# Kernel optimization log

Hardware: AMD Instinct MI355X
Metric: run time of the kernel (lower is better)

## Reference

```python
import jax, jax.numpy as jnp
import numpy as np

ZDIM, NF, H, S, B = 64, 32, 256, 256, 1024


def setup_inputs() -> dict:
    key = jax.random.key(0)
    ks = jax.random.split(key, 8)
    def w(k, shape, fan):
        return (jax.random.normal(k, shape, jnp.float32) / np.sqrt(fan)).astype(jnp.float32)
    return {
        "z": jax.random.normal(ks[0], (B, ZDIM), jnp.float32),
        "W_lat": w(ks[1], (2 * H, ZDIM), ZDIM),
        "b_lat": jnp.zeros((2 * H,), jnp.float32),
        "W_ih": w(ks[2], (4 * H, NF), NF),
        "b_ih": jnp.zeros((4 * H,), jnp.float32),
        "W_hh": w(ks[3], (4 * H, H), H),
        "b_hh": jnp.zeros((4 * H,), jnp.float32),
        "W_out": w(ks[4], (NF, H), H),
        "b_out": jnp.zeros((NF,), jnp.float32),
        "W_sig": w(ks[5], (NF, H * S), H * S),
        "b_sig": jnp.zeros((NF,), jnp.float32),
    }


def reference(z, W_lat, b_lat, W_ih, b_ih, W_hh, b_hh, W_out, b_out, W_sig, b_sig):
    # from_latent: split into initial hidden / cell state
    hc = z @ W_lat.T + b_lat                      # [B, 2H]
    h, c = hc[:, :H], hc[:, H:]
    x = jnp.zeros((z.shape[0], NF), z.dtype)      # initial LSTM input
    bias = b_ih + b_hh                            # fold both LSTM biases

    def step(carry, _):
        h, c, x = carry
        g = x @ W_ih.T + h @ W_hh.T + bias        # [B, 4H]; torch gate order i,f,g,o
        i, f, gg, o = jnp.split(g, 4, axis=-1)
        c = jax.nn.sigmoid(f) * c + jax.nn.sigmoid(i) * jnp.tanh(gg)
        h = jax.nn.sigmoid(o) * jnp.tanh(c)
        x_next = jnp.tanh(h) @ W_out.T + b_out    # activation(Tanh) then from_lstm
        return (h, c, x_next), (h, x_next)

    _, (hs, mus) = jax.lax.scan(step, (h, c, x), None, length=S)
    # mus: [S, B, NF] -> mu: [B, NF, S]
    mu = jnp.transpose(mus, (1, 2, 0))
    # hs: [S, B, H] -> [B, H, S] -> flatten hidden-major, matching torch permute+reshape
    xs = jnp.transpose(hs, (1, 2, 0)).reshape(-1, H * S)
    sigma = jax.nn.softplus(xs @ W_sig.T + b_sig)[:, :, None]   # [B, NF, 1]
    return (mu, sigma)
```

## Files before the change

kernel.cpp:

```cpp
#include <hip/hip_runtime.h>

#define ZDIM 64
#define NF 32
#define HDIM 256
#define SLEN 256
#define BATCH 1024

typedef float f32x4 __attribute__((ext_vector_type(4)));
typedef __bf16 bf16x8 __attribute__((ext_vector_type(8)));

#define MFMA __builtin_amdgcn_mfma_f32_16x16x32_bf16

#define WHH_O 0
#define WIH_O 32768
#define WOUT_O 36864
#define WLAT_O 37888
#define PREP1_N 41984
#define WT_BYTE (1 << 20)
#define HST_BYTE (8 << 20)

__device__ __forceinline__ unsigned short f2bf(float x) {
  union { float f; unsigned int u; } v; v.f = x;
  unsigned int r = (v.u + 0x7FFFu + ((v.u >> 16) & 1u)) >> 16;
  return (unsigned short)r;
}
__device__ __forceinline__ unsigned int pk2(float a, float b) {
  return (unsigned int)f2bf(a) | ((unsigned int)f2bf(b) << 16);
}
__device__ __forceinline__ float sigf(float x) {
  return __fdividef(1.0f, 1.0f + __expf(-x));
}
__device__ __forceinline__ float tanhf_(float x) {
  return 1.0f - __fdividef(2.0f, __expf(2.0f * x) + 1.0f);
}

__global__ void prep_weights(const float* __restrict__ Whh, const float* __restrict__ Wih,
                             const float* __restrict__ Wout, const float* __restrict__ Wlat,
                             uint4* __restrict__ ws) {
  int i = blockIdx.x * 256 + threadIdx.x;
  if (i >= PREP1_N) return;
  int l = i & 63;
  int c16 = l & 15, g4 = l >> 4;
  const float* src;
  if (i < WIH_O) {
    int t = (i >> 6) & 7, j = i >> 9;
    src = Whh + (j * 16 + c16) * 256 + t * 32 + 8 * g4;
  } else if (i < WOUT_O) {
    int ii = i - WIH_O;
    int j = ii >> 6;
    src = Wih + (j * 16 + c16) * 32 + 8 * g4;
  } else if (i < WLAT_O) {
    int ii = i - WOUT_O;
    int t = (ii >> 6) & 7, j = ii >> 9;
    src = Wout + (j * 16 + c16) * 256 + t * 32 + 8 * g4;
  } else {
    int ii = i - WLAT_O;
    int t = (ii >> 6) & 1, j = ii >> 7;
    src = Wlat + (j * 16 + c16) * 64 + t * 32 + 8 * g4;
  }
  uint4 P;
  P.x = pk2(src[0], src[1]);
  P.y = pk2(src[2], src[3]);
  P.z = pk2(src[4], src[5]);
  P.w = pk2(src[6], src[7]);
  ws[i] = P;
}

__global__ void prep_wt(const float* __restrict__ Wsig, unsigned short* __restrict__ Wt) {
  __shared__ float tile[32][257];
  int f = blockIdx.x >> 3, hb = blockIdx.x & 7;
  int tid = threadIdx.x;
  const float* src = Wsig + f * (HDIM * SLEN) + hb * 32 * 256;
#pragma unroll
  for (int i = 0; i < 32; ++i) {
    tile[i][tid] = src[i * 256 + tid];
  }
  __syncthreads();
  int s = tid;
  unsigned short tmp[32];
#pragma unroll
  for (int h = 0; h < 32; ++h) tmp[h] = f2bf(tile[h][s]);
  uint4* dst = (uint4*)(Wt + f * 65536 + s * 256 + hb * 32);
  const uint4* tsrc = (const uint4*)tmp;
#pragma unroll
  for (int j = 0; j < 4; ++j) dst[j] = tsrc[j];
}

__global__ __launch_bounds__(512) void lstm_scan(
    const float* __restrict__ z, const float* __restrict__ b_lat,
    const float* __restrict__ b_ih, const float* __restrict__ b_hh,
    const float* __restrict__ b_out,
    const uint4* __restrict__ ws, unsigned short* __restrict__ hst,
    float* __restrict__ out) {
  __shared__ __align__(16) uint4 wihb[4096];
  __shared__ __align__(16) uint4 woutb[1024];
  __shared__ __align__(16) unsigned short hbuf[2][16][256];
  __shared__ __align__(16) unsigned short thbuf[16][256];
  __shared__ __align__(16) unsigned short xbuf[2][16][32];
  __shared__ __align__(16) float mubuf[16][16][32];
  __shared__ __align__(16) unsigned short zb[16][64];

  const int tid = threadIdx.x;
  const int w = tid >> 6;
  const int l = tid & 63;
  const int c16 = l & 15;
  const int g4 = l >> 4;
  const int r0 = g4 * 4;
  const int wg = blockIdx.x;

  for (int i = tid; i < 4096; i += 512) wihb[i] = ws[WIH_O + i];
  for (int i = tid; i < 1024; i += 512) woutb[i] = ws[WOUT_O + i];

  float biasv[8];
#pragma unroll
  for (int q = 0; q < 8; ++q) {
    int n = (q * 8 + w) * 16 + c16;
    biasv[q] = b_ih[n] + b_hh[n];
  }
  float bo = 0.f;
  if (w < 2) bo = b_out[w * 16 + c16];

  for (int idx = tid; idx < 16 * 64; idx += 512) {
    int m = idx >> 6, k = idx & 63;
    zb[m][k] = f2bf(z[(wg * 16 + m) * 64 + k]);
  }
  xbuf[0][tid >> 5][tid & 31] = 0;
  __syncthreads();

  float cst[2][4];
  {
    bf16x8 za0 = *reinterpret_cast<const bf16x8*>(&zb[c16][8 * g4]);
    bf16x8 za1 = *reinterpret_cast<const bf16x8*>(&zb[c16][32 + 8 * g4]);
    f32x4 a2[4];
#pragma unroll
    for (int q2 = 0; q2 < 4; ++q2) {
      int j = q2 * 8 + w;
      float bl = b_lat[j * 16 + c16];
      f32x4 a = {bl, bl, bl, bl};
      a = MFMA(za0, *reinterpret_cast<const bf16x8*>(ws + WLAT_O + (j * 2 + 0) * 64 + l), a, 0, 0, 0);
      a = MFMA(za1, *reinterpret_cast<const bf16x8*>(ws + WLAT_O + (j * 2 + 1) * 64 + l), a, 0, 0, 0);
      a2[q2] = a;
    }
#pragma unroll
    for (int q2 = 0; q2 < 2; ++q2) {
      int col = q2 * 128 + w * 16 + c16;
#pragma unroll
      for (int v = 0; v < 4; ++v) {
        int rr = r0 + v;
        hbuf[0][rr][col ^ ((rr & 7) << 3)] = f2bf(a2[q2][v]);
      }
    }
#pragma unroll
    for (int p = 0; p < 2; ++p)
#pragma unroll
      for (int v = 0; v < 4; ++v) cst[p][v] = a2[2 + p][v];
  }
  __syncthreads();

  for (int s = 0; s < SLEN; ++s) {
    const int pb = s & 1;
    bf16x8 afr[8];
#pragma unroll
    for (int t = 0; t < 8; ++t) {
      int kb = t * 32 + 8 * g4;
      afr[t] = *reinterpret_cast<const bf16x8*>(&hbuf[pb][c16][kb ^ ((c16 & 7) << 3)]);
    }
    bf16x8 xfr = *reinterpret_cast<const bf16x8*>(&xbuf[pb][c16][8 * g4]);
    f32x4 acc[8];
#pragma unroll
    for (int q = 0; q < 8; ++q) {
      f32x4 a = {biasv[q], biasv[q], biasv[q], biasv[q]};
      a = MFMA(xfr, *reinterpret_cast<const bf16x8*>(&wihb[(q * 8 + w) * 64 + l]), a, 0, 0, 0);
      const uint4* bp = ws + WHH_O + ((q * 8 + w) * 8) * 64 + l;
#pragma unroll
      for (int t = 0; t < 8; ++t)
        a = MFMA(afr[t], *reinterpret_cast<const bf16x8*>(bp + t * 64), a, 0, 0, 0);
      acc[q] = a;
    }

#pragma unroll
    for (int p = 0; p < 2; ++p) {
      const int hcol = p * 128 + w * 16 + c16;
#pragma unroll
      for (int v = 0; v < 4; ++v) {
        float iv = acc[0 + p][v];
        float fv = acc[2 + p][v];
        float gv = acc[4 + p][v];
        float ov = acc[6 + p][v];
        float cc = sigf(fv) * cst[p][v] + sigf(iv) * tanhf_(gv);
        cst[p][v] = cc;
        float hh = sigf(ov) * tanhf_(cc);
        float th = tanhf_(hh);
        int rr = r0 + v;
        int sc = hcol ^ ((rr & 7) << 3);
        hbuf[pb ^ 1][rr][sc] = f2bf(hh);
        thbuf[rr][sc] = f2bf(th);
      }
    }
    __syncthreads();
    if (w < 2) {
      f32x4 xacc = {bo, bo, bo, bo};
#pragma unroll
      for (int t = 0; t < 8; ++t) {
        bf16x8 ta = *reinterpret_cast<const bf16x8*>(
            &thbuf[c16][(t * 32 + 8 * g4) ^ ((c16 & 7) << 3)]);
        xacc = MFMA(ta, *reinterpret_cast<const bf16x8*>(&woutb[(w * 8 + t) * 64 + l]), xacc, 0, 0, 0);
      }
      const int f = w * 16 + c16;
      const int sw = s & 15;
#pragma unroll
      for (int v = 0; v < 4; ++v) {
        int rr = r0 + v;
        float xv = xacc[v];
        xbuf[pb ^ 1][rr][f] = f2bf(xv);
        mubuf[sw][rr][f] = xv;
      }
    } else if (w >= 4) {
      int t4 = tid - 256;
#pragma unroll
      for (int rep = 0; rep < 2; ++rep) {
        int task = t4 + rep * 256;
        int r = task >> 5;
        int h0 = (task & 31) * 8;
        uint4 d = *reinterpret_cast<const uint4*>(&hbuf[pb ^ 1][r][h0 ^ ((r & 7) << 3)]);
        *reinterpret_cast<uint4*>(hst + ((wg * 16 + r) << 16) + (s << 8) + h0) = d;
      }
    }
    __syncthreads();
    if ((s & 15) == 15) {
      int b = tid >> 5, f = tid & 31;
      float* dst = out + ((wg * 16 + b) << 13) + (f << 8) + (s - 15);
#pragma unroll
      for (int j4 = 0; j4 < 4; ++j4) {
        f32x4 vv;
#pragma unroll
        for (int jj = 0; jj < 4; ++jj) vv[jj] = mubuf[j4 * 4 + jj][b][f];
        *reinterpret_cast<f32x4*>(dst + j4 * 4) = vv;
      }
    }
  }
}

__global__ __launch_bounds__(512) void sigma_gemm(
    const unsigned short* __restrict__ hst, const unsigned short* __restrict__ Wt,
    const float* __restrict__ b_sig, float* __restrict__ out) {
  __shared__ float sred[8][16][32];
  const int tid = threadIdx.x;
  const int w = tid >> 6;
  const int l = tid & 63;
  const int c16 = l & 15;
  const int g4 = l >> 4;
  const int wg = blockIdx.x;

  const unsigned short* ap =
      hst + (((wg << 2) + (c16 & 3)) << 16) + ((w * 32) << 8) + (g4 << 3);
  const unsigned short* bp0 = Wt + (c16 << 16) + ((w * 32) << 8) + (g4 << 3);
  const unsigned short* bp1 = Wt + ((16 + c16) << 16) + ((w * 32) << 8) + (g4 << 3);

  f32x4 a0 = {0.f, 0.f, 0.f, 0.f}, a1 = {0.f, 0.f, 0.f, 0.f};
#pragma unroll 8
  for (int kk = 0; kk < 256; ++kk) {
    int off = ((kk >> 3) << 8) + ((kk & 7) << 5);
    bf16x8 av = *reinterpret_cast<const bf16x8*>(ap + off);
    a0 = MFMA(av, *reinterpret_cast<const bf16x8*>(bp0 + off), a0, 0, 0, 0);
    a1 = MFMA(av, *reinterpret_cast<const bf16x8*>(bp1 + off), a1, 0, 0, 0);
  }
#pragma unroll
  for (int v = 0; v < 4; ++v) {
    sred[w][g4 * 4 + v][c16] = a0[v];
    sred[w][g4 * 4 + v][16 + c16] = a1[v];
  }
  __syncthreads();
  int b = tid >> 5, f = tid & 31;
  if (b < 4) {
    float acc = b_sig[f];
#pragma unroll
    for (int ww = 0; ww < 8; ++ww) acc += sred[ww][b][f];
    float sp = fmaxf(acc, 0.0f) + log1pf(__expf(-fabsf(acc)));
    out[BATCH * NF * SLEN + ((wg << 2) + b) * NF + f] = sp;
  }
}

extern "C" void kernel_launch(void* const* d_in, const int* in_sizes, int n_in,
                              void* d_out, int out_size, void* d_ws, size_t ws_size,
                              hipStream_t stream) {
  (void)in_sizes; (void)n_in; (void)out_size; (void)ws_size;
  const float* z     = (const float*)d_in[0];
  const float* W_lat = (const float*)d_in[1];
  const float* b_lat = (const float*)d_in[2];
  const float* W_ih  = (const float*)d_in[3];
  const float* b_ih  = (const float*)d_in[4];
  const float* W_hh  = (const float*)d_in[5];
  const float* b_hh  = (const float*)d_in[6];
  const float* W_out = (const float*)d_in[7];
  const float* b_out = (const float*)d_in[8];
  const float* W_sig = (const float*)d_in[9];
  const float* b_sig = (const float*)d_in[10];
  uint4* ws = (uint4*)d_ws;
  unsigned short* Wt  = (unsigned short*)((char*)d_ws + WT_BYTE);
  unsigned short* hst = (unsigned short*)((char*)d_ws + HST_BYTE);
  float* out = (float*)d_out;

  prep_weights<<<(PREP1_N + 255) / 256, 256, 0, stream>>>(W_hh, W_ih, W_out, W_lat, ws);
  prep_wt<<<256, 256, 0, stream>>>(W_sig, Wt);
  lstm_scan<<<64, 512, 0, stream>>>(z, b_lat, b_ih, b_hh, b_out, ws, hst, out);
  sigma_gemm<<<256, 512, 0, stream>>>(hst, Wt, b_sig, out);
}
```

Baseline: 3.255 ms.

## Keep W_hh resident in registers and LDS, prefetch the remainder from global

Repartitions the recurrent weight W_hh per wave: three gate tiles are pinned in VGPRs, two are staged in LDS, and the remaining three are streamed from global memory with software prefetch overlapping the MFMAs. The LDS previously used for W_ih/W_out staging and the mu staging buffer is freed, so W_ih and W_out are now read from global each step and mu is written straight to the output with strided scalar stores. The aim is to cut the per-step global/L2 traffic for W_hh on the latency-bound serial scan. The cost is heavy register pressure, which the launch_bounds(512,2) hint tightens further, plus less coalesced mu stores.

Measured after the change: 3.485 ms. +7.1%, slower.

```diff
diff --git a/kernel.cpp b/kernel.cpp
--- a/kernel.cpp
+++ b/kernel.cpp
@@ -1,6 +1,5 @@
 #include <hip/hip_runtime.h>
 
-#define ZDIM 64
 #define NF 32
 #define HDIM 256
 #define SLEN 256
@@ -8,6 +7,8 @@
 
 typedef float f32x4 __attribute__((ext_vector_type(4)));
 typedef __bf16 bf16x8 __attribute__((ext_vector_type(8)));
+typedef unsigned int u32x4 __attribute__((ext_vector_type(4)));
+typedef unsigned short u16;
 
 #define MFMA __builtin_amdgcn_mfma_f32_16x16x32_bf16
 
@@ -16,13 +17,12 @@
 #define WOUT_O 36864
 #define WLAT_O 37888
 #define PREP1_N 41984
-#define WT_BYTE (1 << 20)
-#define HST_BYTE (8 << 20)
-
-__device__ __forceinline__ unsigned short f2bf(float x) {
+#define WT_BYTE (1u << 20)
+#define HST_BYTE (8u << 20)
+
+__device__ __forceinline__ u16 f2bf(float x) {
   union { float f; unsigned int u; } v; v.f = x;
-  unsigned int r = (v.u + 0x7FFFu + ((v.u >> 16) & 1u)) >> 16;
-  return (unsigned short)r;
+  return (u16)((v.u + 0x7FFFu + ((v.u >> 16) & 1u)) >> 16);
 }
 __device__ __forceinline__ unsigned int pk2(float a, float b) {
   return (unsigned int)f2bf(a) | ((unsigned int)f2bf(b) << 16);
@@ -72,9 +72,7 @@
   int tid = threadIdx.x;
   const float* src = Wsig + f * (HDIM * SLEN) + hb * 32 * 256;
 #pragma unroll
-  for (int i = 0; i < 32; ++i) {
-    tile[i][tid] = src[i * 256 + tid];
-  }
+  for (int i = 0; i < 32; ++i) tile[i][tid] = src[i * 256 + tid];
   __syncthreads();
   int s = tid;
   unsigned short tmp[32];
@@ -86,30 +84,38 @@
   for (int j = 0; j < 4; ++j) dst[j] = tsrc[j];
 }
 
-__global__ __launch_bounds__(512) void lstm_scan(
+__global__ __launch_bounds__(512, 2) void lstm_scan(
     const float* __restrict__ z, const float* __restrict__ b_lat,
     const float* __restrict__ b_ih, const float* __restrict__ b_hh,
     const float* __restrict__ b_out,
     const uint4* __restrict__ ws, unsigned short* __restrict__ hst,
     float* __restrict__ out) {
-  __shared__ __align__(16) uint4 wihb[4096];
-  __shared__ __align__(16) uint4 woutb[1024];
-  __shared__ __align__(16) unsigned short hbuf[2][16][256];
-  __shared__ __align__(16) unsigned short thbuf[16][256];
-  __shared__ __align__(16) unsigned short xbuf[2][16][32];
-  __shared__ __align__(16) float mubuf[16][16][32];
-  __shared__ __align__(16) unsigned short zb[16][64];
-
-  const int tid = threadIdx.x;
-  const int w = tid >> 6;
-  const int l = tid & 63;
-  const int c16 = l & 15;
-  const int g4 = l >> 4;
-  const int r0 = g4 * 4;
+  __shared__ __align__(16) uint4 whhl[8192];
+  __shared__ __align__(16) u16 hbuf[2][16][256];
+  __shared__ __align__(16) u16 thbuf[16][256];
+  __shared__ __align__(16) u16 xbuf[2][16][32];
+
+  const int tid = threadIdx.x, w = tid >> 6, l = tid & 63;
+  const int c16 = l & 15, g4 = l >> 4, r0 = g4 * 4;
   const int wg = blockIdx.x;
-
-  for (int i = tid; i < 4096; i += 512) wihb[i] = ws[WIH_O + i];
-  for (int i = tid; i < 1024; i += 512) woutb[i] = ws[WOUT_O + i];
+  const int swz = (c16 & 7) << 3;
+
+  for (int i = tid; i < 8192; i += 512) {
+    int l_ = i & 63, kt = (i >> 6) & 7, qq = (i >> 9) & 1, w_ = i >> 10;
+    whhl[i] = ws[WHH_O + (((4 + qq) * 8 + w_) * 8 + kt) * 64 + l_];
+  }
+
+  u32x4 wp[3][8];
+#pragma unroll
+  for (int qi = 0; qi < 3; ++qi)
+#pragma unroll
+    for (int kt = 0; kt < 8; ++kt)
+      wp[qi][kt] = __builtin_bit_cast(u32x4, ws[WHH_O + ((qi * 8 + w) * 8 + kt) * 64 + l]);
+#pragma unroll
+  for (int qi = 0; qi < 3; ++qi)
+#pragma unroll
+    for (int kt = 0; kt < 8; ++kt)
+      asm volatile("" : "+v"(wp[qi][kt]));
 
   float biasv[8];
 #pragma unroll
@@ -117,20 +123,17 @@
     int n = (q * 8 + w) * 16 + c16;
     biasv[q] = b_ih[n] + b_hh[n];
   }
-  float bo = 0.f;
-  if (w < 2) bo = b_out[w * 16 + c16];
-
-  for (int idx = tid; idx < 16 * 64; idx += 512) {
-    int m = idx >> 6, k = idx & 63;
-    zb[m][k] = f2bf(z[(wg * 16 + m) * 64 + k]);
-  }
+  float bo = (w < 2) ? b_out[w * 16 + c16] : 0.f;
+
+  for (int idx = tid; idx < 1024; idx += 512)
+    thbuf[idx >> 6][idx & 63] = f2bf(z[(wg * 16 + (idx >> 6)) * 64 + (idx & 63)]);
   xbuf[0][tid >> 5][tid & 31] = 0;
   __syncthreads();
 
   float cst[2][4];
   {
-    bf16x8 za0 = *reinterpret_cast<const bf16x8*>(&zb[c16][8 * g4]);
-    bf16x8 za1 = *reinterpret_cast<const bf16x8*>(&zb[c16][32 + 8 * g4]);
+    bf16x8 za0 = *reinterpret_cast<const bf16x8*>(&thbuf[c16][8 * g4]);
+    bf16x8 za1 = *reinterpret_cast<const bf16x8*>(&thbuf[c16][32 + 8 * g4]);
     f32x4 a2[4];
 #pragma unroll
     for (int q2 = 0; q2 < 4; ++q2) {
@@ -157,26 +160,55 @@
   }
   __syncthreads();
 
+  const uint4* bs3 = ws + WHH_O + ((3 * 8 + w) * 8) * 64 + l;
+  const uint4* bs6 = ws + WHH_O + ((6 * 8 + w) * 8) * 64 + l;
+  const uint4* bs7 = ws + WHH_O + ((7 * 8 + w) * 8) * 64 + l;
+
   for (int s = 0; s < SLEN; ++s) {
     const int pb = s & 1;
-    bf16x8 afr[8];
-#pragma unroll
-    for (int t = 0; t < 8; ++t) {
-      int kb = t * 32 + 8 * g4;
-      afr[t] = *reinterpret_cast<const bf16x8*>(&hbuf[pb][c16][kb ^ ((c16 & 7) << 3)]);
+    uint4 pf[12];
+#pragma unroll
+    for (int kt = 0; kt < 4; ++kt) {
+      pf[kt * 3 + 0] = bs3[kt * 64];
+      pf[kt * 3 + 1] = bs6[kt * 64];
+      pf[kt * 3 + 2] = bs7[kt * 64];
+    }
+    f32x4 acc[8];
+#pragma unroll
+    for (int q = 0; q < 8; ++q) acc[q] = (f32x4){biasv[q], biasv[q], biasv[q], biasv[q]};
+#pragma unroll
+    for (int kt = 0; kt < 8; ++kt) {
+      bf16x8 afr = *reinterpret_cast<const bf16x8*>(&hbuf[pb][c16][(kt * 32 + 8 * g4) ^ swz]);
+      acc[0] = MFMA(afr, __builtin_bit_cast(bf16x8, wp[0][kt]), acc[0], 0, 0, 0);
+      acc[1] = MFMA(afr, __builtin_bit_cast(bf16x8, wp[1][kt]), acc[1], 0, 0, 0);
+      acc[2] = MFMA(afr, __builtin_bit_cast(bf16x8, wp[2][kt]), acc[2], 0, 0, 0);
+      acc[4] = MFMA(afr, *reinterpret_cast<const bf16x8*>(&whhl[((w * 2 + 0) * 8 + kt) * 64 + l]), acc[4], 0, 0, 0);
+      acc[5] = MFMA(afr, *reinterpret_cast<const bf16x8*>(&whhl[((w * 2 + 1) * 8 + kt) * 64 + l]), acc[5], 0, 0, 0);
+    }
+    bf16x8 wihv[8];
+#pragma unroll
+    for (int q = 0; q < 8; ++q)
+      wihv[q] = *reinterpret_cast<const bf16x8*>(ws + WIH_O + (q * 8 + w) * 64 + l);
+#pragma unroll
+    for (int kt = 0; kt < 4; ++kt) {
+      bf16x8 afr = *reinterpret_cast<const bf16x8*>(&hbuf[pb][c16][(kt * 32 + 8 * g4) ^ swz]);
+      acc[3] = MFMA(afr, __builtin_bit_cast(bf16x8, pf[kt * 3 + 0]), acc[3], 0, 0, 0);
+      acc[6] = MFMA(afr, __builtin_bit_cast(bf16x8, pf[kt * 3 + 1]), acc[6], 0, 0, 0);
+      acc[7] = MFMA(afr, __builtin_bit_cast(bf16x8, pf[kt * 3 + 2]), acc[7], 0, 0, 0);
+      pf[kt * 3 + 0] = bs3[(4 + kt) * 64];
+      pf[kt * 3 + 1] = bs6[(4 + kt) * 64];
+      pf[kt * 3 + 2] = bs7[(4 + kt) * 64];
+    }
+#pragma unroll
+    for (int kt = 4; kt < 8; ++kt) {
+      bf16x8 afr = *reinterpret_cast<const bf16x8*>(&hbuf[pb][c16][(kt * 32 + 8 * g4) ^ swz]);
+      acc[3] = MFMA(afr, __builtin_bit_cast(bf16x8, pf[(kt - 4) * 3 + 0]), acc[3], 0, 0, 0);
+      acc[6] = MFMA(afr, __builtin_bit_cast(bf16x8, pf[(kt - 4) * 3 + 1]), acc[6], 0, 0, 0);
+      acc[7] = MFMA(afr, __builtin_bit_cast(bf16x8, pf[(kt - 4) * 3 + 2]), acc[7], 0, 0, 0);
     }
     bf16x8 xfr = *reinterpret_cast<const bf16x8*>(&xbuf[pb][c16][8 * g4]);
-    f32x4 acc[8];
-#pragma unroll
-    for (int q = 0; q < 8; ++q) {
-      f32x4 a = {biasv[q], biasv[q], biasv[q], biasv[q]};
-      a = MFMA(xfr, *reinterpret_cast<const bf16x8*>(&wihb[(q * 8 + w) * 64 + l]), a, 0, 0, 0);
-      const uint4* bp = ws + WHH_O + ((q * 8 + w) * 8) * 64 + l;
-#pragma unroll
-      for (int t = 0; t < 8; ++t)
-        a = MFMA(afr[t], *reinterpret_cast<const bf16x8*>(bp + t * 64), a, 0, 0, 0);
-      acc[q] = a;
-    }
+#pragma unroll
+    for (int q = 0; q < 8; ++q) acc[q] = MFMA(xfr, wihv[q], acc[q], 0, 0, 0);
 
 #pragma unroll
     for (int p = 0; p < 2; ++p) {
@@ -202,18 +234,17 @@
       f32x4 xacc = {bo, bo, bo, bo};
 #pragma unroll
       for (int t = 0; t < 8; ++t) {
-        bf16x8 ta = *reinterpret_cast<const bf16x8*>(
-            &thbuf[c16][(t * 32 + 8 * g4) ^ ((c16 & 7) << 3)]);
-        xacc = MFMA(ta, *reinterpret_cast<const bf16x8*>(&woutb[(w * 8 + t) * 64 + l]), xacc, 0, 0, 0);
+        bf16x8 ta = *reinterpret_cast<const bf16x8*>(&thbuf[c16][(t * 32 + 8 * g4) ^ swz]);
+        bf16x8 wov = *reinterpret_cast<const bf16x8*>(ws + WOUT_O + (w * 8 + t) * 64 + l);
+        xacc = MFMA(ta, wov, xacc, 0, 0, 0);
       }
       const int f = w * 16 + c16;
-      const int sw = s & 15;
 #pragma unroll
       for (int v = 0; v < 4; ++v) {
         int rr = r0 + v;
         float xv = xacc[v];
         xbuf[pb ^ 1][rr][f] = f2bf(xv);
-        mubuf[sw][rr][f] = xv;
+        out[(wg * 16 + rr) * (NF * SLEN) + f * SLEN + s] = xv;
       }
     } else if (w >= 4) {
       int t4 = tid - 256;
@@ -227,17 +258,6 @@
       }
     }
     __syncthreads();
-    if ((s & 15) == 15) {
-      int b = tid >> 5, f = tid & 31;
-      float* dst = out + ((wg * 16 + b) << 13) + (f << 8) + (s - 15);
-#pragma unroll
-      for (int j4 = 0; j4 < 4; ++j4) {
-        f32x4 vv;
-#pragma unroll
-        for (int jj = 0; jj < 4; ++jj) vv[jj] = mubuf[j4 * 4 + jj][b][f];
-        *reinterpret_cast<f32x4*>(dst + j4 * 4) = vv;
-      }
-    }
   }
 }
 
@@ -296,9 +316,10 @@
   const float* b_out = (const float*)d_in[8];
   const float* W_sig = (const float*)d_in[9];
   const float* b_sig = (const float*)d_in[10];
-  uint4* ws = (uint4*)d_ws;
-  unsigned short* Wt  = (unsigned short*)((char*)d_ws + WT_BYTE);
-  unsigned short* hst = (unsigned short*)((char*)d_ws + HST_BYTE);
+  char* wsb = (char*)d_ws;
+  uint4* ws = (uint4*)wsb;
+  unsigned short* Wt  = (unsigned short*)(wsb + WT_BYTE);
+  unsigned short* hst = (unsigned short*)(wsb + HST_BYTE);
   float* out = (float*)d_out;
 
   prep_weights<<<(PREP1_N + 255) / 256, 256, 0, stream>>>(W_hh, W_ih, W_out, W_lat, ws);
```
